# Performance work log

Measured on AMD Instinct MI355X. Metric: run time of the kernel, lower is better.

The kernel has to match this reference:

```python
import jax, jax.numpy as jnp
import numpy as np
import math

B, C, BINS, W = 2, 8, 1024, 512
HEADS = 16
HD = BINS // HEADS          # 64 head dim
ROT = BINS // HEADS // 2    # 32 rotated dims
EXP = 4
EPS = 1e-5
MAX_FREQ = 10.0


def setup_inputs() -> dict:
    key = jax.random.key(0)
    ks = jax.random.split(key, 8)
    def u(k, shape, fan_in):
        lim = 1.0 / math.sqrt(fan_in)
        return jax.random.uniform(k, shape, jnp.float32, -lim, lim)
    return {
        "x": jax.random.normal(ks[0], (B, C, BINS, W), jnp.float32),
        "norm1_w": jnp.ones((BINS,), jnp.float32),
        "norm1_b": jnp.zeros((BINS,), jnp.float32),
        # 'pixel' rotary init: linspace(1, max_freq/2, dim//2) * pi (learned)
        "rot_freqs": jnp.linspace(1.0, MAX_FREQ / 2, ROT // 2, dtype=jnp.float32) * math.pi,
        "q_w": u(ks[1], (C, BINS, BINS), BINS),
        "out_w": u(ks[2], (C, BINS, BINS), BINS),
        "norm2_w": jnp.ones((BINS,), jnp.float32),
        "norm2_b": jnp.zeros((BINS,), jnp.float32),
        "lin1_w": u(ks[3], (C, BINS * EXP, BINS), BINS),
        "lin2_w": u(ks[4], (C, BINS, BINS * EXP), BINS * EXP),
    }


def _mlin(x, w):
    # x: [b,c,f_in,w]; w: [c,f_out,f_in] -> [b,c,f_out,w]
    return jnp.einsum('bcfw,cgf->bcgw', x, w)


def _frame_norm(x, w, b):
    # LayerNorm over the bins axis (axis=2) of [b,c,bins,w]
    m = jnp.mean(x, axis=2, keepdims=True)
    v = jnp.var(x, axis=2, keepdims=True)
    xn = (x - m) * jax.lax.rsqrt(v + EPS)
    return xn * w[:, None] + b[:, None]


def _rotate(q, cos, sin):
    # q: [b,c,h,w,d]; rotate first ROT dims with interleaved-pair rotate_half
    q1, q2 = q[..., :ROT], q[..., ROT:]
    qp = q1.reshape(*q1.shape[:-1], ROT // 2, 2)
    rh = jnp.stack([-qp[..., 1], qp[..., 0]], axis=-1).reshape(q1.shape)
    return jnp.concatenate([q1 * cos + rh * sin, q2], axis=-1)


def _attention(x, rot_freqs, q_w, out_w):
    b, c, bins, w = x.shape
    # faithful to source: q, k, v ALL use q_proj
    y = _mlin(x, q_w)  # [b,c,bins,w]
    # -> [b,c,h,w,d]
    y = y.transpose(0, 1, 3, 2).reshape(b, c, w, HEADS, HD).transpose(0, 1, 3, 2, 4)
    # rotary angles: t * freqs, repeat-interleaved x2 -> [w, ROT]
    t = jnp.arange(w, dtype=jnp.float32)
    ang = jnp.repeat(t[:, None] * rot_freqs[None, :], 2, axis=-1)
    cos, sin = jnp.cos(ang), jnp.sin(ang)
    q = _rotate(y, cos, sin)
    k = _rotate(y, cos, sin)
    v = y
    # NOTE: source scales by 1/sqrt(h) where h == bins (spectral height)
    scores = jnp.einsum('bchwd,bchud->bchwu', q, k) / math.sqrt(bins)
    a = jnp.einsum('bchwu,bchud->bchwd', jax.nn.softmax(scores, axis=-1), v)
    # [b,c,h,w,d] -> [b,c,bins,w]
    a = a.transpose(0, 1, 3, 2, 4).reshape(b, c, w, bins).transpose(0, 1, 3, 2)
    return _mlin(a, out_w)


def reference(x, norm1_w, norm1_b, rot_freqs, q_w, out_w,
              norm2_w, norm2_b, lin1_w, lin2_w):
    z = _frame_norm(x, norm1_w, norm1_b)
    z = _attention(z, rot_freqs, q_w, out_w)
    x = x + z  # dropout=0 -> identity
    z = _frame_norm(x, norm2_w, norm2_b)
    z = _mlin(jax.nn.gelu(_mlin(z, lin1_w), approximate=False), lin2_w)
    return x + z
```

## Files before the change

### kernel.cpp

```cpp
#include <hip/hip_runtime.h>
#include <math.h>

#define BB 2
#define CCH 8
#define BINS 1024
#define WW 512
#define HEADS 16
#define HD 64
#define ROTD 32
#define EXPF 4
#define NXE 8388608L
#define NTW 32

typedef unsigned short ushortT;
typedef short bf16x8 __attribute__((ext_vector_type(8)));
typedef float f32x4 __attribute__((ext_vector_type(4)));

__device__ __forceinline__ ushortT f2bf(float f) {
    unsigned int u = __float_as_uint(f);
    u = (u + 0x7FFF + ((u >> 16) & 1)) >> 16;
    return (ushortT)u;
}
__device__ __forceinline__ float bf2f(ushortT h) {
    return __uint_as_float(((unsigned int)h) << 16);
}
__device__ __forceinline__ float geluf(float x) {
    return 0.5f * x * (1.f + erff(x * 0.70710678118654752f));
}
__device__ __forceinline__ void gl_lds16(const ushortT* g, ushortT* l) {
    __builtin_amdgcn_global_load_lds(
        (const __attribute__((address_space(1))) unsigned int*)g,
        (__attribute__((address_space(3))) unsigned int*)l, 16, 0, 0);
}

__global__ __launch_bounds__(1024)
void normT_k(const float* __restrict__ X, const float* __restrict__ wgt,
             const float* __restrict__ bia, ushortT* __restrict__ YT)
{
    __shared__ float tile[NTW][BINS + 1];
    __shared__ float red0[32][NTW], red1[32][NTW];
    __shared__ float ms[NTW], is[NTW];
    const int bc = blockIdx.x >> 4;
    const int w0 = (blockIdx.x & 15) * NTW;
    const int tid = threadIdx.x;
    const int w  = tid & (NTW - 1);
    const int fy = tid >> 5;
    const float* Xb = X + (long)bc * BINS * WW + w0;
    float s = 0.f, s2 = 0.f;
    for (int f = fy; f < BINS; f += 32) {
        float v = Xb[(long)f * WW + w];
        s += v; s2 += v * v;
        tile[w][f] = v;
    }
    red0[fy][w] = s; red1[fy][w] = s2;
    __syncthreads();
    if (tid < NTW) {
        float ss = 0.f, qq = 0.f;
        #pragma unroll
        for (int j = 0; j < 32; ++j) { ss += red0[j][tid]; qq += red1[j][tid]; }
        float m = ss * (1.f / BINS);
        float var = qq * (1.f / BINS) - m * m;
        ms[tid] = m; is[tid] = rsqrtf(var + 1e-5f);
    }
    __syncthreads();
    const int w2 = tid >> 5;
    const int c  = tid & 31;
    float m = ms[w2], inv = is[w2];
    ushortT* Yb = YT + ((long)bc * WW + w0 + w2) * BINS;
    #pragma unroll
    for (int jj = 0; jj < 4; ++jj) {
        int f0 = jj * 256 + c * 8;
        union { ushortT h[8]; uint4 v; } r;
        #pragma unroll
        for (int e = 0; e < 8; ++e) {
            int f = f0 + e;
            float v = (tile[w2][f] - m) * inv * wgt[f] + bia[f];
            r.h[e] = f2bf(v);
        }
        *(uint4*)&Yb[f0] = r.v;
    }
}

__global__ void rope_tab_k(const float* __restrict__ freqs,
                           float* __restrict__ cosT, float* __restrict__ sinT)
{
    int idx = blockIdx.x * 256 + threadIdx.x;
    if (idx >= WW * 16) return;
    int w = idx >> 4, i = idx & 15;
    float ang = (float)w * freqs[i];
    cosT[idx] = cosf(ang);
    sinT[idx] = sinf(ang);
}

__global__ __launch_bounds__(256)
void ropeB_k(const ushortT* __restrict__ yT, const float* __restrict__ cosT,
             const float* __restrict__ sinT, ushortT* __restrict__ rotT)
{
    long e0 = ((long)blockIdx.x * 256 + threadIdx.x) * 8;
    if (e0 >= NXE) return;
    int g0 = (int)(e0 & 1023);
    int w  = (int)((e0 >> 10) & 511);
    int d0 = g0 & 63;
    union { uint4 v; ushortT h8[8]; } in, ov;
    in.v = *(const uint4*)&yT[e0];
    if (d0 >= ROTD) {
        *(uint4*)&rotT[e0] = in.v;
        return;
    }
    #pragma unroll
    for (int j = 0; j < 8; j += 2) {
        int i = (d0 + j) >> 1;
        float c = cosT[w * 16 + i], s = sinT[w * 16 + i];
        float a = bf2f(in.h8[j]), b = bf2f(in.h8[j + 1]);
        ov.h8[j]     = f2bf(a * c - b * s);
        ov.h8[j + 1] = f2bf(b * c + a * s);
    }
    *(uint4*)&rotT[e0] = ov.v;
}

__global__ __launch_bounds__(256)
void mattn_k(const ushortT* __restrict__ rotT, const ushortT* __restrict__ yT,
             ushortT* __restrict__ oT)
{
    __shared__ ushortT Qs[64 * 64];
    __shared__ ushortT Ks[64 * 64];
    __shared__ ushortT Vs[64 * 72];
    __shared__ ushortT Ps[64 * 72];
    const int z = blockIdx.y;
    const int bc = z >> 4, h = z & 15;
    const int wq0 = blockIdx.x * 64;
    const int tid = threadIdx.x;
    const int wv = tid >> 6, l = tid & 63;
    const int lr = l & 15, lk = l >> 4;
    const long hbase = (long)bc * WW * 1024 + h * 64;

    #pragma unroll
    for (int p = 0; p < 2; ++p) {
        int r0 = p * 32 + wv * 8;
        int row = r0 + (l >> 3);
        int gs = (l & 7) ^ (row & 7);
        gl_lds16(rotT + hbase + (long)(wq0 + row) * 1024 + gs * 8, Qs + r0 * 64);
    }

    f32x4 oacc[4] = {};
    float mrow[4] = {-INFINITY, -INFINITY, -INFINITY, -INFINITY};
    float lrow[4] = {0.f, 0.f, 0.f, 0.f};

    for (int u0 = 0; u0 < WW; u0 += 64) {
        #pragma unroll
        for (int p = 0; p < 2; ++p) {
            int r0 = p * 32 + wv * 8;
            int row = r0 + (l >> 3);
            int gs = (l & 7) ^ (row & 7);
            gl_lds16(rotT + hbase + (long)(u0 + row) * 1024 + gs * 8, Ks + r0 * 64);
        }
        #pragma unroll
        for (int rep = 0; rep < 2; ++rep) {
            int ch = rep * 4 + wv;
            union { uint4 v; ushortT h8[8]; } tmp;
            tmp.v = *(const uint4*)(yT + hbase + (long)(u0 + l) * 1024 + ch * 8);
            #pragma unroll
            for (int j = 0; j < 8; ++j)
                Vs[(ch * 8 + j) * 72 + l] = tmp.h8[j];
        }
        __syncthreads();

        f32x4 sacc[4] = {};
        #pragma unroll
        for (int ko = 0; ko < 2; ++ko) {
            int ar = wv * 16 + lr;
            bf16x8 aq = *(const bf16x8*)&Qs[ar * 64 + (((ko * 4) + lk) ^ (ar & 7)) * 8];
            #pragma unroll
            for (int f = 0; f < 4; ++f) {
                int br = f * 16 + lr;
                bf16x8 bk = *(const bf16x8*)&Ks[br * 64 + (((ko * 4) + lk) ^ (br & 7)) * 8];
                sacc[f] = __builtin_amdgcn_mfma_f32_16x16x32_bf16(aq, bk, sacc[f], 0, 0, 0);
            }
        }

        #pragma unroll
        for (int rg = 0; rg < 4; ++rg) {
            float s0 = sacc[0][rg] * (1.f / 32.f);
            float s1 = sacc[1][rg] * (1.f / 32.f);
            float s2 = sacc[2][rg] * (1.f / 32.f);
            float s3 = sacc[3][rg] * (1.f / 32.f);
            float mx = fmaxf(fmaxf(s0, s1), fmaxf(s2, s3));
            mx = fmaxf(mx, __shfl_xor(mx, 1));
            mx = fmaxf(mx, __shfl_xor(mx, 2));
            mx = fmaxf(mx, __shfl_xor(mx, 4));
            mx = fmaxf(mx, __shfl_xor(mx, 8));
            float mnew = fmaxf(mrow[rg], mx);
            float al = __expf(mrow[rg] - mnew);
            float p0 = __expf(s0 - mnew), p1 = __expf(s1 - mnew);
            float p2 = __expf(s2 - mnew), p3 = __expf(s3 - mnew);
            float rs = p0 + p1 + p2 + p3;
            rs += __shfl_xor(rs, 1);
            rs += __shfl_xor(rs, 2);
            rs += __shfl_xor(rs, 4);
            rs += __shfl_xor(rs, 8);
            lrow[rg] = lrow[rg] * al + rs;
            mrow[rg] = mnew;
            oacc[0][rg] *= al; oacc[1][rg] *= al;
            oacc[2][rg] *= al; oacc[3][rg] *= al;
            int prow = wv * 16 + lk * 4 + rg;
            Ps[prow * 72 +  0 + lr] = f2bf(p0);
            Ps[prow * 72 + 16 + lr] = f2bf(p1);
            Ps[prow * 72 + 32 + lr] = f2bf(p2);
            Ps[prow * 72 + 48 + lr] = f2bf(p3);
        }
        asm volatile("s_waitcnt lgkmcnt(0)" ::: "memory");

        #pragma unroll
        for (int ko = 0; ko < 2; ++ko) {
            int ar = wv * 16 + lr;
            bf16x8 ap = *(const bf16x8*)&Ps[ar * 72 + ko * 32 + lk * 8];
            #pragma unroll
            for (int f = 0; f < 4; ++f) {
                bf16x8 bv = *(const bf16x8*)&Vs[(f * 16 + lr) * 72 + ko * 32 + lk * 8];
                oacc[f] = __builtin_amdgcn_mfma_f32_16x16x32_bf16(ap, bv, oacc[f], 0, 0, 0);
            }
        }
        __syncthreads();
    }

    #pragma unroll
    for (int rg = 0; rg < 4; ++rg) {
        float inv = 1.f / lrow[rg];
        int w = wq0 + wv * 16 + lk * 4 + rg;
        long b2 = (long)bc * WW * 1024 + (long)w * 1024 + h * 64;
        #pragma unroll
        for (int f = 0; f < 4; ++f)
            oT[b2 + f * 16 + lr] = f2bf(oacc[f][rg] * inv);
    }
}

template<bool HASRES, bool GELUF, bool TRANSOUT>
__global__ __launch_bounds__(256)
void fgemm_k(const float* __restrict__ A, long sA, int aMod,
             const ushortT* __restrict__ B, long sB,
             void* __restrict__ Cp, long sC,
             const float* __restrict__ R, long sR,
             int M, int N, int K, int gx, int gy)
{
    __shared__ ushortT smem[2 * 8192];
    ushortT* As = smem;
    ushortT* Bs = smem + 8192;
    const int nwg = gridDim.x;
    const int bid = blockIdx.x;
    const int lid = (bid & 7) * (nwg >> 3) + (bid >> 3);
    const int x = lid % gx;
    const int y = (lid / gx) % gy;
    const int z = lid / (gx * gy);
    const float*   Ab = A + (long)(z % aMod) * sA + (long)y * 128 * K;
    const ushortT* Bb = B + (long)z * sB + (long)x * 128 * K;
    const int tid = threadIdx.x;
    const int wv = tid >> 6, l = tid & 63;
    const int lrow = l & 15, lk = l >> 4;
    const int mb = (wv >> 1) * 64, nb = (wv & 1) * 64;
    const int arow = tid >> 3, agrp = tid & 7;
    f32x4 acc[4][4] = {};
    float4 a0[4], a1[4];
    const int NT = K >> 6;

    auto fetchA = [&](int k0) {
        #pragma unroll
        for (int c = 0; c < 4; ++c) {
            const float* src = Ab + (long)(arow + c * 32) * K + k0 + agrp * 8;
            a0[c] = *(const float4*)src;
            a1[c] = *(const float4*)(src + 4);
        }
    };
    auto commitA = [&]() {
        #pragma unroll
        for (int c = 0; c < 4; ++c) {
            int row = arow + c * 32;
            union { ushortT h[8]; uint4 v; } r;
            r.h[0] = f2bf(a0[c].x); r.h[1] = f2bf(a0[c].y);
            r.h[2] = f2bf(a0[c].z); r.h[3] = f2bf(a0[c].w);
            r.h[4] = f2bf(a1[c].x); r.h[5] = f2bf(a1[c].y);
            r.h[6] = f2bf(a1[c].z); r.h[7] = f2bf(a1[c].w);
            *(uint4*)&As[row * 64 + ((agrp ^ (row & 7)) << 3)] = r.v;
        }
    };
    auto stageB = [&](int k0) {
        #pragma unroll
        for (int t = 0; t < 4; ++t) {
            int r0 = wv * 32 + t * 8;
            int row = r0 + (l >> 3);
            int gs = (l & 7) ^ (row & 7);
            gl_lds16(Bb + (long)row * K + k0 + gs * 8, Bs + r0 * 64);
        }
    };
    auto compute = [&]() {
        #pragma unroll
        for (int ko = 0; ko < 2; ++ko) {
            bf16x8 af[4], bg[4];
            #pragma unroll
            for (int i = 0; i < 4; ++i) {
                int ra = mb + i * 16 + lrow;
                af[i] = *(const bf16x8*)&As[ra * 64 + ((lk + ko * 4) ^ (ra & 7)) * 8];
                int rb = nb + i * 16 + lrow;
                bg[i] = *(const bf16x8*)&Bs[rb * 64 + ((lk + ko * 4) ^ (rb & 7)) * 8];
            }
            #pragma unroll
            for (int i = 0; i < 4; ++i)
                #pragma unroll
                for (int j = 0; j < 4; ++j)
                    acc[i][j] = __builtin_amdgcn_mfma_f32_16x16x32_bf16(
                        af[i], bg[j], acc[i][j], 0, 0, 0);
        }
    };

    fetchA(0);
    for (int t = 0; t < NT; ++t) {
        __builtin_amdgcn_s_barrier();
        __builtin_amdgcn_sched_barrier(0);
        stageB(t << 6);
        __builtin_amdgcn_sched_barrier(0);
        commitA();
        if (t + 1 < NT) {
            fetchA((t + 1) << 6);
            __builtin_amdgcn_sched_barrier(0);
            asm volatile("s_waitcnt vmcnt(8) lgkmcnt(0)" ::: "memory");
        } else {
            __builtin_amdgcn_sched_barrier(0);
            asm volatile("s_waitcnt vmcnt(0) lgkmcnt(0)" ::: "memory");
        }
        __builtin_amdgcn_s_barrier();
        __builtin_amdgcn_sched_barrier(0);
        compute();
    }

    const int m0g = y * 128 + mb, n0g = x * 128 + nb;
    if (!TRANSOUT) {
        float* Cf = (float*)Cp + (long)z * sC;
        #pragma unroll
        for (int i = 0; i < 4; ++i)
            #pragma unroll
            for (int j = 0; j < 4; ++j)
                #pragma unroll
                for (int rg = 0; rg < 4; ++rg) {
                    long m = m0g + i * 16 + lk * 4 + rg;
                    long n = n0g + j * 16 + lrow;
                    float v = acc[i][j][rg];
                    if (GELUF) v = geluf(v);
                    if (HASRES) v += R[(long)z * sR + m * N + n];
                    Cf[m * N + n] = v;
                }
    } else {
        ushortT* Ts = smem + wv * 4096;
        __syncthreads();
        #pragma unroll
        for (int i = 0; i < 4; ++i)
            #pragma unroll
            for (int j = 0; j < 4; ++j)
                #pragma unroll
                for (int rg = 0; rg < 4; ++rg) {
                    int ml = i * 16 + lk * 4 + rg;
                    int nl = j * 16 + lrow;
                    float v = acc[i][j][rg];
                    if (GELUF) v = geluf(v);
                    Ts[nl * 64 + (((ml >> 3) ^ (nl & 7)) << 3) + (ml & 7)] = f2bf(v);
                }
        __syncthreads();
        ushortT* CT = (ushortT*)Cp + (long)z * sC;
        #pragma unroll
        for (int p = 0; p < 8; ++p) {
            int nl = p * 8 + (l >> 3), mc = l & 7;
            uint4 d = *(const uint4*)&Ts[nl * 64 + ((mc ^ (nl & 7)) << 3)];
            *(uint4*)&CT[(long)(n0g + nl) * M + m0g + mc * 8] = d;
        }
    }
}

extern "C" void kernel_launch(void* const* d_in, const int* in_sizes, int n_in,
                              void* d_out, int out_size, void* d_ws, size_t ws_size,
                              hipStream_t stream)
{
    const float* x    = (const float*)d_in[0];
    const float* n1w  = (const float*)d_in[1];
    const float* n1b  = (const float*)d_in[2];
    const float* freqs= (const float*)d_in[3];
    const float* qw   = (const float*)d_in[4];
    const float* ow   = (const float*)d_in[5];
    const float* n2w  = (const float*)d_in[6];
    const float* n2b  = (const float*)d_in[7];
    const float* l1w  = (const float*)d_in[8];
    const float* l2w  = (const float*)d_in[9];
    float* out = (float*)d_out;
    char* wsb  = (char*)d_ws;
    const long MB = 1L << 20;

    ushortT* znT  = (ushortT*)(wsb +   0 * MB);
    ushortT* yT   = (ushortT*)(wsb +  16 * MB);
    ushortT* rotT = (ushortT*)(wsb +  32 * MB);
    ushortT* CfT  = (ushortT*)(wsb +  48 * MB);
    ushortT* zn2T = (ushortT*)(wsb +  64 * MB);
    ushortT* h1T  = (ushortT*)(wsb +  80 * MB);
    float*   cosT = (float*)  (wsb + 144 * MB);
    float*   sinT = cosT + WW * 16;

    rope_tab_k<<<32, 256, 0, stream>>>(freqs, cosT, sinT);

    normT_k<<<BB * CCH * 16, 1024, 0, stream>>>(x, n1w, n1b, znT);

    fgemm_k<false, false, true><<<512, 256, 0, stream>>>(
        qw,  (long)BINS * BINS, CCH,
        znT, (long)WW * BINS,
        yT,  (long)WW * BINS,
        nullptr, 0, BINS, WW, BINS, 4, 8);

    ropeB_k<<<4096, 256, 0, stream>>>(yT, cosT, sinT, rotT);

    mattn_k<<<dim3(8, 256), 256, 0, stream>>>(rotT, yT, CfT);

    fgemm_k<true, false, false><<<512, 256, 0, stream>>>(
        ow,  (long)BINS * BINS, CCH,
        CfT, (long)WW * BINS,
        out, (long)BINS * WW,
        x,   (long)BINS * WW, BINS, WW, BINS, 4, 8);

    normT_k<<<BB * CCH * 16, 1024, 0, stream>>>(out, n2w, n2b, zn2T);

    fgemm_k<false, true, true><<<2048, 256, 0, stream>>>(
        l1w,  (long)BINS * EXPF * BINS, CCH,
        zn2T, (long)WW * BINS,
        h1T,  (long)WW * BINS * EXPF,
        nullptr, 0, BINS * EXPF, WW, BINS, 4, 32);

    fgemm_k<true, false, false><<<512, 256, 0, stream>>>(
        l2w, (long)BINS * BINS * EXPF, CCH,
        h1T, (long)WW * BINS * EXPF,
        out, (long)BINS * WW,
        out, (long)BINS * WW, BINS, WW, BINS * EXPF, 4, 8);
}
```

Measured before the change: 436.4 us.

## Fuse RoPE into Q-projection epilogue, packed bf16 convert, simplify pipeline sync

Removes the standalone RoPE kernel and applies the rotary rotation in the transposed-output epilogue of the Q-projection GEMM, writing both the plain and rotated tensors. This saves one full read and write of the 16 MB activation. The fp32-to-bf16 packing of A tiles now uses the hardware v_cvt_pk_bf16_f32 instruction in place of manual rounding. The hand-tuned barrier/waitcnt pipeline is replaced with plain __syncthreads, which may lose the overlap between the global loads and the MFMA compute.

```diff
diff --git a/kernel.cpp b/kernel.cpp
--- a/kernel.cpp
+++ b/kernel.cpp
@@ -23,6 +23,11 @@
 }
 __device__ __forceinline__ float bf2f(ushortT h) {
     return __uint_as_float(((unsigned int)h) << 16);
+}
+__device__ __forceinline__ unsigned int cvtpk(float lo, float hi) {
+    unsigned int r;
+    asm("v_cvt_pk_bf16_f32 %0, %1, %2" : "=v"(r) : "v"(lo), "v"(hi));
+    return r;
 }
 __device__ __forceinline__ float geluf(float x) {
     return 0.5f * x * (1.f + erff(x * 0.70710678118654752f));
@@ -90,32 +95,6 @@
     float ang = (float)w * freqs[i];
     cosT[idx] = cosf(ang);
     sinT[idx] = sinf(ang);
-}
-
-__global__ __launch_bounds__(256)
-void ropeB_k(const ushortT* __restrict__ yT, const float* __restrict__ cosT,
-             const float* __restrict__ sinT, ushortT* __restrict__ rotT)
-{
-    long e0 = ((long)blockIdx.x * 256 + threadIdx.x) * 8;
-    if (e0 >= NXE) return;
-    int g0 = (int)(e0 & 1023);
-    int w  = (int)((e0 >> 10) & 511);
-    int d0 = g0 & 63;
-    union { uint4 v; ushortT h8[8]; } in, ov;
-    in.v = *(const uint4*)&yT[e0];
-    if (d0 >= ROTD) {
-        *(uint4*)&rotT[e0] = in.v;
-        return;
-    }
-    #pragma unroll
-    for (int j = 0; j < 8; j += 2) {
-        int i = (d0 + j) >> 1;
-        float c = cosT[w * 16 + i], s = sinT[w * 16 + i];
-        float a = bf2f(in.h8[j]), b = bf2f(in.h8[j + 1]);
-        ov.h8[j]     = f2bf(a * c - b * s);
-        ov.h8[j + 1] = f2bf(b * c + a * s);
-    }
-    *(uint4*)&rotT[e0] = ov.v;
 }
 
 __global__ __launch_bounds__(256)
@@ -234,12 +213,14 @@
     }
 }
 
-template<bool HASRES, bool GELUF, bool TRANSOUT>
+template<bool HASRES, bool GELUF, bool TRANSOUT, bool ROPE>
 __global__ __launch_bounds__(256)
 void fgemm_k(const float* __restrict__ A, long sA, int aMod,
              const ushortT* __restrict__ B, long sB,
              void* __restrict__ Cp, long sC,
              const float* __restrict__ R, long sR,
+             ushortT* __restrict__ Crot,
+             const float* __restrict__ cosT, const float* __restrict__ sinT,
              int M, int N, int K, int gx, int gy)
 {
     __shared__ ushortT smem[2 * 8192];
@@ -274,12 +255,12 @@
         #pragma unroll
         for (int c = 0; c < 4; ++c) {
             int row = arow + c * 32;
-            union { ushortT h[8]; uint4 v; } r;
-            r.h[0] = f2bf(a0[c].x); r.h[1] = f2bf(a0[c].y);
-            r.h[2] = f2bf(a0[c].z); r.h[3] = f2bf(a0[c].w);
-            r.h[4] = f2bf(a1[c].x); r.h[5] = f2bf(a1[c].y);
-            r.h[6] = f2bf(a1[c].z); r.h[7] = f2bf(a1[c].w);
-            *(uint4*)&As[row * 64 + ((agrp ^ (row & 7)) << 3)] = r.v;
+            uint4 v;
+            v.x = cvtpk(a0[c].x, a0[c].y);
+            v.y = cvtpk(a0[c].z, a0[c].w);
+            v.z = cvtpk(a1[c].x, a1[c].y);
+            v.w = cvtpk(a1[c].z, a1[c].w);
+            *(uint4*)&As[row * 64 + ((agrp ^ (row & 7)) << 3)] = v;
         }
     };
     auto stageB = [&](int k0) {
@@ -313,21 +294,11 @@
 
     fetchA(0);
     for (int t = 0; t < NT; ++t) {
-        __builtin_amdgcn_s_barrier();
-        __builtin_amdgcn_sched_barrier(0);
+        if (t > 0) __syncthreads();
         stageB(t << 6);
-        __builtin_amdgcn_sched_barrier(0);
         commitA();
-        if (t + 1 < NT) {
-            fetchA((t + 1) << 6);
-            __builtin_amdgcn_sched_barrier(0);
-            asm volatile("s_waitcnt vmcnt(8) lgkmcnt(0)" ::: "memory");
-        } else {
-            __builtin_amdgcn_sched_barrier(0);
-            asm volatile("s_waitcnt vmcnt(0) lgkmcnt(0)" ::: "memory");
-        }
-        __builtin_amdgcn_s_barrier();
-        __builtin_amdgcn_sched_barrier(0);
+        if (t + 1 < NT) fetchA((t + 1) << 6);
+        __syncthreads();
         compute();
     }
 
@@ -368,7 +339,28 @@
         for (int p = 0; p < 8; ++p) {
             int nl = p * 8 + (l >> 3), mc = l & 7;
             uint4 d = *(const uint4*)&Ts[nl * 64 + ((mc ^ (nl & 7)) << 3)];
-            *(uint4*)&CT[(long)(n0g + nl) * M + m0g + mc * 8] = d;
+            int wg = n0g + nl;
+            int g0 = m0g + mc * 8;
+            *(uint4*)&CT[(long)wg * M + g0] = d;
+            if (ROPE) {
+                ushortT* RT = Crot + (long)z * sC;
+                int d0 = g0 & 63;
+                if (d0 >= ROTD) {
+                    *(uint4*)&RT[(long)wg * M + g0] = d;
+                } else {
+                    union { uint4 v; ushortT h8[8]; } in, ov;
+                    in.v = d;
+                    #pragma unroll
+                    for (int j = 0; j < 8; j += 2) {
+                        int i2 = (d0 + j) >> 1;
+                        float cc = cosT[wg * 16 + i2], ss = sinT[wg * 16 + i2];
+                        float a = bf2f(in.h8[j]), b = bf2f(in.h8[j + 1]);
+                        ov.h8[j]     = f2bf(a * cc - b * ss);
+                        ov.h8[j + 1] = f2bf(b * cc + a * ss);
+                    }
+                    *(uint4*)&RT[(long)wg * M + g0] = ov.v;
+                }
+            }
         }
     }
 }
@@ -404,33 +396,39 @@
 
     normT_k<<<BB * CCH * 16, 1024, 0, stream>>>(x, n1w, n1b, znT);
 
-    fgemm_k<false, false, true><<<512, 256, 0, stream>>>(
+    fgemm_k<false, false, true, true><<<512, 256, 0, stream>>>(
         qw,  (long)BINS * BINS, CCH,
         znT, (long)WW * BINS,
         yT,  (long)WW * BINS,
-        nullptr, 0, BINS, WW, BINS, 4, 8);
-
-    ropeB_k<<<4096, 256, 0, stream>>>(yT, cosT, sinT, rotT);
+        nullptr, 0,
+        rotT, cosT, sinT,
+        BINS, WW, BINS, 4, 8);
 
     mattn_k<<<dim3(8, 256), 256, 0, stream>>>(rotT, yT, CfT);
 
-    fgemm_k<true, false, false><<<512, 256, 0, stream>>>(
+    fgemm_k<true, false, false, false><<<512, 256, 0, stream>>>(
         ow,  (long)BINS * BINS, CCH,
         CfT, (long)WW * BINS,
         out, (long)BINS * WW,
-        x,   (long)BINS * WW, BINS, WW, BINS, 4, 8);
+        x,   (long)BINS * WW,
+        nullptr, nullptr, nullptr,
+        BINS, WW, BINS, 4, 8);
 
     normT_k<<<BB * CCH * 16, 1024, 0, stream>>>(out, n2w, n2b, zn2T);
 
-    fgemm_k<false, true, true><<<2048, 256, 0, stream>>>(
+    fgemm_k<false, true, true, false><<<2048, 256, 0, stream>>>(
         l1w,  (long)BINS * EXPF * BINS, CCH,
         zn2T, (long)WW * BINS,
         h1T,  (long)WW * BINS * EXPF,
-        nullptr, 0, BINS * EXPF, WW, BINS, 4, 32);
-
-    fgemm_k<true, false, false><<<512, 256, 0, stream>>>(
+        nullptr, 0,
+        nullptr, nullptr, nullptr,
+        BINS * EXPF, WW, BINS, 4, 32);
+
+    fgemm_k<true, false, false, false><<<512, 256, 0, stream>>>(
         l2w, (long)BINS * BINS * EXPF, CCH,
         h1T, (long)WW * BINS * EXPF,
         out, (long)BINS * WW,
-        out, (long)BINS * WW, BINS, WW, BINS * EXPF, 4, 8);
-}
+        out, (long)BINS * WW,
+        nullptr, nullptr, nullptr,
+        BINS, WW, BINS * EXPF, 4, 8);
+}
```

Measured after the change: 439.2 us. No clear change (+0.7%).
